# Performance work log

Hardware: AMD Instinct MI355X
Metric: run time of the kernel (lower is better)

## Reference

```python
import jax, jax.numpy as jnp
import numpy as np

B, C, D = 16384, 512, 512
EXT = 2
H = C * EXT
TAU = 1.0          # temperature_train
STEP = 0.05        # langevin_step_size
NOISE = 0.1        # langevin_noise
STEPS = 32         # langevin_steps


def setup_inputs() -> dict:
    key = jax.random.key(0)
    ks = jax.random.split(key, 8)
    s_in = 1.0 / np.sqrt(D)
    s_h = 1.0 / np.sqrt(H)
    return {
        'x': jax.random.normal(ks[0], (B, D), jnp.float32),
        'vanilla_components': jnp.abs(jax.random.normal(ks[1], (C, D), jnp.float32) * 0.1),
        'e_sp': jax.random.normal(ks[2], (C * D,), jnp.float32) * 0.1,
        'W1e': jax.random.normal(ks[3], (D, H), jnp.float32) * s_in,
        'b1e': jnp.zeros((H,), jnp.float32),
        'W2e': jax.random.normal(ks[4], (H, C), jnp.float32) * s_h,
        'b2e': jnp.zeros((C,), jnp.float32),
        'W1r': jax.random.normal(ks[5], (D, H), jnp.float32) * s_in,
        'b1r': jnp.zeros((H,), jnp.float32),
        'W2r': jax.random.normal(ks[6], (H, C), jnp.float32) * s_h,
        'b2r': jnp.zeros((C,), jnp.float32),
    }


def _langevin_gate(e, key):
    """Langevin MCMC on latent u with quadratic energy E(u)=0.5||u||^2 + <e,u>.
    Returns selection probability sigmoid(-u/tau)."""
    def step(u, k):
        grad = u + e  # dE/du
        u = u - STEP * grad + NOISE * jax.random.normal(k, u.shape, u.dtype)
        return u, None
    u, _ = jax.lax.scan(step, jnp.zeros_like(e), jax.random.split(key, STEPS))
    return jax.nn.sigmoid(-u / TAU)


def reference(x, vanilla_components, e_sp, W1e, b1e, W2e, b2e, W1r, b1r, W2r, b2r):
    k1, k2 = jax.random.split(jax.random.key(42))
    # non-negative components
    comps = jnp.abs(vanilla_components)  # [C, D]
    # fixed energy-based sparsity mask over component entries
    p_sp = _langevin_gate(e_sp, k1).reshape(C, D)
    comps = comps * p_sp
    # dynamic per-sample component selection energies via MLP
    h = jax.nn.relu(x @ W1e + b1e)          # [B, H]
    e_dyn = h @ W2e + b2e                   # [B, C]
    gate = _langevin_gate(e_dyn, k2)        # [B, C] soft gates (train mode)
    hr = jax.nn.relu(x @ W1r + b1r)         # [B, H]
    conc = (hr @ W2r + b2r) * gate          # [B, C]
    # aggregate: (concentration * components).sum over components -> [B, D]
    return conc @ comps
```

## Files before the change

kernel.cpp:

```cpp
#include <hip/hip_runtime.h>
#include <hip/hip_bf16.h>
#include <stdint.h>

#define Bn 16384
#define Cn 512
#define Dn 512
#define Hn 1024

#define A32 0.80628851f

typedef __attribute__((ext_vector_type(8))) short bf16x8;
typedef __attribute__((ext_vector_type(4))) float f32x4;
typedef __attribute__((ext_vector_type(2))) float f32x2;

__device__ __forceinline__ ushort f2bf(float f) {
  uint32_t u = __float_as_uint(f);
  return (ushort)((u + 0x7fffu + ((u >> 16) & 1u)) >> 16);
}
__device__ __forceinline__ float b2f(ushort u) {
  return __uint_as_float((uint32_t)u << 16);
}

typedef __attribute__((address_space(3))) uint32_t lds_u32_t;
typedef const __attribute__((address_space(1))) uint32_t glb_u32_t;
__device__ __forceinline__ void gload16(const ushort* g, ushort* l) {
  __builtin_amdgcn_global_load_lds((glb_u32_t*)g, (lds_u32_t*)l, 16, 0, 0);
}

constexpr uint32_t crotl(uint32_t v, int s) {
  return (v << s) | (v >> (32 - s));
}
struct TFOut { uint32_t w0, w1; };
constexpr TFOut ctf(uint32_t k0, uint32_t k1, uint32_t x0, uint32_t x1) {
  const uint32_t ks[3] = {k0, k1, k0 ^ k1 ^ 0x1BD11BDAu};
  const int rot[8] = {13, 15, 26, 6, 17, 29, 16, 24};
  uint32_t a = x0 + k0, b = x1 + k1;
  for (int g = 0; g < 5; ++g) {
    for (int i = 0; i < 4; ++i) {
      int r = rot[(g & 1) * 4 + i];
      a += b; b = crotl(b, r); b ^= a;
    }
    a += ks[(g + 1) % 3];
    b += ks[(g + 2) % 3] + (uint32_t)(g + 1);
  }
  return {a, b};
}
struct KeySched { uint32_t s[64]; uint32_t d[64]; };
constexpr KeySched make_keys() {
  KeySched K{};
  TFOut k1 = ctf(0u, 42u, 0u, 0u);
  TFOut k2 = ctf(0u, 42u, 0u, 1u);
  for (uint32_t t = 0; t < 32; ++t) {
    TFOut ws = ctf(k1.w0, k1.w1, 0u, t);
    K.s[2 * t] = ws.w0; K.s[2 * t + 1] = ws.w1;
    TFOut wd = ctf(k2.w0, k2.w1, 0u, t);
    K.d[2 * t] = wd.w0; K.d[2 * t + 1] = wd.w1;
  }
  return K;
}
__constant__ KeySched KS = make_keys();

__device__ __forceinline__ uint32_t rotl32(uint32_t v, int s) {
  return __builtin_rotateleft32(v, (uint32_t)s);
}
__device__ __forceinline__ uint32_t tf_xor(uint32_t K0, uint32_t K1,
                                           uint32_t KX, uint32_t j) {
  uint32_t a = K0, b = K1 + j;
#define TR(r) { a += b; b = rotl32(b, (r)); b ^= a; }
  TR(13) TR(15) TR(26) TR(6)   a += K1; b += KX + 1u;
  TR(17) TR(29) TR(16) TR(24)  a += KX; b += K0 + 2u;
  TR(13) TR(15) TR(26) TR(6)   a += K0; b += K1 + 3u;
  TR(17) TR(29) TR(16) TR(24)  a += K1; b += KX + 4u;
  TR(13) TR(15) TR(26) TR(6)   a += KX; b += K0 + 5u;
#undef TR
  return a ^ b;
}

__device__ __forceinline__ float bits_to_normal(uint32_t bits) {
  float f = __uint_as_float((bits >> 9) | 0x3f800000u) - 1.0f;
  float x = f * 2.0f - 0x1.fffffep-1f;
  float w = -__logf(1.0f - x * x);
  float p;
  if (w < 5.0f) {
    w -= 2.5f;
    p =            2.81022636e-08f;
    p = fmaf(p, w, 3.43273939e-07f);
    p = fmaf(p, w, -3.5233877e-06f);
    p = fmaf(p, w, -4.39150654e-06f);
    p = fmaf(p, w, 0.00021858087f);
    p = fmaf(p, w, -0.00125372503f);
    p = fmaf(p, w, -0.00417768164f);
    p = fmaf(p, w, 0.246640727f);
    p = fmaf(p, w, 1.50140941f);
  } else {
    w = sqrtf(w) - 3.0f;
    p =            -0.000200214257f;
    p = fmaf(p, w, 0.000100950558f);
    p = fmaf(p, w, 0.00134934322f);
    p = fmaf(p, w, -0.00367342844f);
    p = fmaf(p, w, 0.00573950773f);
    p = fmaf(p, w, -0.0076224613f);
    p = fmaf(p, w, 0.00943887047f);
    p = fmaf(p, w, 1.00167406f);
    p = fmaf(p, w, 2.83297682f);
  }
  return 0x1.6a09e6p+0f * (p * x);
}

__device__ __forceinline__ void z_block(ushort* __restrict__ Z, uint32_t zidx) {
  const uint32_t j0 = (zidx * 256u + threadIdx.x) * 2u;
  const uint32_t j1 = j0 + 1u;
  float z0 = 0.0f, z1 = 0.0f;
#pragma unroll 4
  for (int t = 0; t < 32; ++t) {
    const uint32_t K0 = KS.d[2 * t], K1 = KS.d[2 * t + 1];
    const uint32_t KX = K0 ^ K1 ^ 0x1BD11BDAu;
    uint32_t a0 = K0, b0 = K1 + j0;
    uint32_t a1 = K0, b1 = K1 + j1;
#define R2(r)                                                  \
    a0 += b0; a1 += b1;                                        \
    b0 = rotl32(b0, (r)); b1 = rotl32(b1, (r));                \
    b0 ^= a0; b1 ^= a1;
#define I2(p, q) a0 += (p); a1 += (p); b0 += (q); b1 += (q);
    R2(13) R2(15) R2(26) R2(6)  I2(K1, KX + 1u)
    R2(17) R2(29) R2(16) R2(24) I2(KX, K0 + 2u)
    R2(13) R2(15) R2(26) R2(6)  I2(K0, K1 + 3u)
    R2(17) R2(29) R2(16) R2(24) I2(K1, KX + 4u)
    R2(13) R2(15) R2(26) R2(6)  I2(KX, K0 + 5u)
#undef R2
#undef I2
    uint32_t s0 = a0 ^ b0, s1 = a1 ^ b1;
    float f0 = __uint_as_float((s0 >> 9) | 0x3f800000u) - 1.0f;
    float f1 = __uint_as_float((s1 >> 9) | 0x3f800000u) - 1.0f;
    float x0 = f0 * 2.0f - 0x1.fffffep-1f;
    float x1 = f1 * 2.0f - 0x1.fffffep-1f;
    float w0 = fminf(-__logf(fmaf(-x0, x0, 1.0f)), 5.0f) - 2.5f;
    float w1 = fminf(-__logf(fmaf(-x1, x1, 1.0f)), 5.0f) - 2.5f;
    f32x2 X = {x0, x1}, W = {w0, w1};
    f32x2 P = {2.81022636e-08f, 2.81022636e-08f};
    P = __builtin_elementwise_fma(P, W, (f32x2){3.43273939e-07f, 3.43273939e-07f});
    P = __builtin_elementwise_fma(P, W, (f32x2){-3.5233877e-06f, -3.5233877e-06f});
    P = __builtin_elementwise_fma(P, W, (f32x2){-4.39150654e-06f, -4.39150654e-06f});
    P = __builtin_elementwise_fma(P, W, (f32x2){0.00021858087f, 0.00021858087f});
    P = __builtin_elementwise_fma(P, W, (f32x2){-0.00125372503f, -0.00125372503f});
    P = __builtin_elementwise_fma(P, W, (f32x2){-0.00417768164f, -0.00417768164f});
    P = __builtin_elementwise_fma(P, W, (f32x2){0.246640727f, 0.246640727f});
    P = __builtin_elementwise_fma(P, W, (f32x2){1.50140941f, 1.50140941f});
    f32x2 Q = (P * X) * (f32x2){0.14142135f, 0.14142135f};
    z0 = fmaf(0.95f, z0, Q.x);
    z1 = fmaf(0.95f, z1, Q.y);
  }
  *(ushort2*)(Z + j0) = make_ushort2(f2bf(z0), f2bf(z1));
}

__device__ __forceinline__ void transpose_tile(
    const float* __restrict__ in, ushort* __restrict__ out,
    int N, int K, int tIdx, float T[32][33]) {
  const int ntn = N / 32;
  const int tk = tIdx / ntn, tn = tIdx % ntn;
  const int tx = threadIdx.x & 31, ty = threadIdx.x >> 5;
  const int k0 = tk * 32, n0 = tn * 32;
#pragma unroll
  for (int r = 0; r < 32; r += 8)
    T[ty + r][tx] = in[(size_t)(k0 + ty + r) * N + n0 + tx];
  __syncthreads();
#pragma unroll
  for (int r = 0; r < 32; r += 8)
    out[(size_t)(n0 + ty + r) * K + k0 + tx] = f2bf(T[tx][ty + r]);
}

__device__ __forceinline__ void smask_block(
    const float* __restrict__ vc, const float* __restrict__ e_sp,
    ushort* __restrict__ compsT, int g) {
  uint32_t jj = (uint32_t)g * 256 + threadIdx.x;
  uint32_t c = jj & (Cn - 1), d = jj >> 9;
  uint32_t ridx = c * Dn + d;
  float e = e_sp[ridx];
  float u = 0.0f;
#pragma unroll 4
  for (int t = 0; t < 32; ++t) {
    const uint32_t K0 = KS.s[2 * t], K1 = KS.s[2 * t + 1];
    uint32_t s = tf_xor(K0, K1, K0 ^ K1 ^ 0x1BD11BDAu, ridx);
    float n = bits_to_normal(s);
    u = (u - 0.05f * (u + e)) + 0.1f * n;
  }
  float gt = 1.0f / (1.0f + __expf(u));
  compsT[jj] = f2bf(fabsf(vc[ridx]) * gt);
}

__global__ __launch_bounds__(256) void k_prep_z(
    const float* __restrict__ x, ushort* __restrict__ x_bf,
    const float* __restrict__ W1e, ushort* __restrict__ W1eT,
    const float* __restrict__ W2e, ushort* __restrict__ W2eT,
    const float* __restrict__ W1r, ushort* __restrict__ W1rT,
    const float* __restrict__ W2r, ushort* __restrict__ W2rT,
    const float* __restrict__ vc, const float* __restrict__ e_sp,
    ushort* __restrict__ compsT, ushort* __restrict__ Zd) {
  __shared__ float T[32][33];
  const int pos = blockIdx.x;
  if ((pos % 5) == 4) {
    z_block(Zd, (uint32_t)(pos / 5));
    return;
  }
  const int p = (pos / 5) * 4 + (pos % 5);
  if (p < 8192) {
    int i = (p * 256 + threadIdx.x) * 4;
    float4 v = *(const float4*)(x + i);
    *(ushort4*)(x_bf + i) =
        make_ushort4(f2bf(v.x), f2bf(v.y), f2bf(v.z), f2bf(v.w));
  } else if (p < 8704) {
    transpose_tile(W1e, W1eT, Hn, Dn, p - 8192, T);
  } else if (p < 9216) {
    transpose_tile(W2e, W2eT, Cn, Hn, p - 8704, T);
  } else if (p < 9728) {
    transpose_tile(W1r, W1rT, Hn, Dn, p - 9216, T);
  } else if (p < 10240) {
    transpose_tile(W2r, W2rT, Cn, Hn, p - 9728, T);
  } else {
    smask_block(vc, e_sp, compsT, p - 10240);
  }
}

__device__ __forceinline__ void gemm_core(
    const ushort* __restrict__ A, const ushort* __restrict__ WT,
    int m0, int n0, int LD, int K,
    ushort* __restrict__ AsL, ushort* __restrict__ BsL,
    f32x4 acc[4][4]) {
  const int t = threadIdx.x;
  const int wave = t >> 6, lane = t & 63;
  const int row = t >> 2;
  const int col8 = ((t & 3) << 3) ^ (((t >> 3) & 3) << 3);
  const int wm = (wave >> 1) << 6, wn = (wave & 1) << 6;
  const int quad = lane >> 4, l15 = lane & 15;
  const int rc = (quad << 3) ^ (((l15 >> 1) & 3) << 3);

  const ushort* ga0 = A  + (size_t)(m0 + row) * LD + col8;
  const ushort* ga1 = A  + (size_t)(m0 + 64 + row) * LD + col8;
  const ushort* gb0 = WT + (size_t)(n0 + row) * LD + col8;
  const ushort* gb1 = WT + (size_t)(n0 + 64 + row) * LD + col8;
  ushort* la0 = AsL + wave * 512;
  ushort* la1 = AsL + 2048 + wave * 512;
  ushort* lb0 = BsL + wave * 512;
  ushort* lb1 = BsL + 2048 + wave * 512;

  for (int k0 = 0; k0 < K; k0 += 32) {
    gload16(ga0 + k0, la0);
    gload16(ga1 + k0, la1);
    gload16(gb0 + k0, lb0);
    gload16(gb1 + k0, lb1);
    __syncthreads();
    bf16x8 af[4], bfr[4];
#pragma unroll
    for (int i = 0; i < 4; ++i) {
      af[i]  = *(const bf16x8*)&AsL[(wm + i * 16 + l15) * 32 + rc];
      bfr[i] = *(const bf16x8*)&BsL[(wn + i * 16 + l15) * 32 + rc];
    }
#pragma unroll
    for (int i = 0; i < 4; ++i)
#pragma unroll
      for (int j = 0; j < 4; ++j)
        acc[i][j] = __builtin_amdgcn_mfma_f32_16x16x32_bf16(af[i], bfr[j],
                                                            acc[i][j], 0, 0, 0);
    __syncthreads();
  }
}

__device__ __forceinline__ void gemm_tile_bf(
    const ushort* __restrict__ A, const ushort* __restrict__ WT,
    const float* __restrict__ bias, ushort* __restrict__ Out, int g,
    ushort* AsL, ushort* BsL) {
  const int n0 = (g & 7) * 128, m0 = (g >> 3) * 128;
  const int t = threadIdx.x;
  const int wave = t >> 6, lane = t & 63;
  const int wm = (wave >> 1) << 6, wn = (wave & 1) << 6;
  const int quad = lane >> 4, l15 = lane & 15;
  f32x4 acc[4][4] = {};
  gemm_core(A, WT, m0, n0, Dn, Dn, AsL, BsL, acc);
#pragma unroll
  for (int i = 0; i < 4; ++i)
#pragma unroll
    for (int j = 0; j < 4; ++j) {
      const int col = n0 + wn + j * 16 + l15;
      const float bv = bias[col];
#pragma unroll
      for (int r = 0; r < 4; ++r) {
        const int row = m0 + wm + i * 16 + quad * 4 + r;
        Out[(size_t)row * Hn + col] = f2bf(fmaxf(acc[i][j][r] + bv, 0.0f));
      }
    }
}

__global__ __launch_bounds__(256) void k_g13_z(
    const ushort* __restrict__ x_bf,
    const ushort* __restrict__ W1eT, const float* __restrict__ b1e,
    ushort* __restrict__ h,
    const ushort* __restrict__ W1rT, const float* __restrict__ b1r,
    ushort* __restrict__ hr, ushort* __restrict__ Zd) {
  __shared__ ushort AsL[4096];
  __shared__ ushort BsL[4096];
  const int pos = blockIdx.x;
  if (pos % 3) {
    z_block(Zd, 2816u + (uint32_t)(pos / 3) * 2u + (uint32_t)(pos % 3) - 1u);
    return;
  }
  const int gg = pos / 3;
  const int g = gg >> 1;
  if (gg & 1)
    gemm_tile_bf(x_bf, W1rT, b1r, hr, g, AsL, BsL);
  else
    gemm_tile_bf(x_bf, W1eT, b1e, h, g, AsL, BsL);
}

__device__ __forceinline__ void gemm_tile_f32out(
    const ushort* __restrict__ A, const ushort* __restrict__ WT,
    const float* __restrict__ bias, float* __restrict__ Out,
    int m0, int n0, ushort* AsL, ushort* BsL) {
  const int t = threadIdx.x;
  const int wave = t >> 6, lane = t & 63;
  const int wm = (wave >> 1) << 6, wn = (wave & 1) << 6;
  const int quad = lane >> 4, l15 = lane & 15;
  f32x4 acc[4][4] = {};
  gemm_core(A, WT, m0, n0, Hn, Hn, AsL, BsL, acc);
#pragma unroll
  for (int i = 0; i < 4; ++i)
#pragma unroll
    for (int j = 0; j < 4; ++j) {
      const int col = n0 + wn + j * 16 + l15;
      const float bv = bias[col];
#pragma unroll
      for (int r = 0; r < 4; ++r) {
        const int row = m0 + wm + i * 16 + quad * 4 + r;
        Out[(size_t)row * Cn + col] = acc[i][j][r] + bv;
      }
    }
}

__global__ __launch_bounds__(256) void k_e_z(
    const ushort* __restrict__ h, const ushort* __restrict__ W2eT,
    const float* __restrict__ b2e, float* __restrict__ e_out,
    ushort* __restrict__ Zd) {
  __shared__ ushort AsL[4096];
  __shared__ ushort BsL[4096];
  const int pos = blockIdx.x;
  if ((pos % 10) == 0) {
    const int tg = pos / 10;
    gemm_tile_f32out(h, W2eT, b2e, e_out, (tg >> 2) * 128, (tg & 3) * 128,
                     AsL, BsL);
  } else {
    z_block(Zd, 6912u + (uint32_t)(pos / 10) * 9u + (uint32_t)(pos % 10) - 1u);
  }
}

__global__ __launch_bounds__(256) void k_r_z(
    const ushort* __restrict__ hr, const ushort* __restrict__ W2rT,
    const float* __restrict__ b2r, float* __restrict__ cr_out,
    ushort* __restrict__ Zd) {
  __shared__ ushort AsL[4096];
  __shared__ ushort BsL[4096];
  const int pos = blockIdx.x;
  if (pos >= 5120) {
    z_block(Zd, 16128u + (uint32_t)(pos - 5120));
    return;
  }
  if ((pos % 10) == 0) {
    const int tg = pos / 10;
    gemm_tile_f32out(hr, W2rT, b2r, cr_out, (tg >> 2) * 128, (tg & 3) * 128,
                     AsL, BsL);
  } else {
    z_block(Zd, 11520u + (uint32_t)(pos / 10) * 9u + (uint32_t)(pos % 10) - 1u);
  }
}

__global__ __launch_bounds__(256) void k_gate(
    const float* __restrict__ e, const float* __restrict__ cr,
    ushort* __restrict__ Z) {
  const size_t i = ((size_t)blockIdx.x * 256u + threadIdx.x) * 8u;
  uint4 zv = *(const uint4*)(Z + i);
  ushort zs[8];
  *(uint4*)zs = zv;
  float ee[8], cc[8];
  *(float4*)(ee)     = *(const float4*)(e + i);
  *(float4*)(ee + 4) = *(const float4*)(e + i + 4);
  *(float4*)(cc)     = *(const float4*)(cr + i);
  *(float4*)(cc + 4) = *(const float4*)(cr + i + 4);
  ushort os[8];
#pragma unroll
  for (int k = 0; k < 8; ++k) {
    float z = b2f(zs[k]);
    float g = 1.0f / (1.0f + __expf(z - A32 * ee[k]));
    os[k] = f2bf(cc[k] * g);
  }
  *(uint4*)(Z + i) = *(uint4*)os;
}

__global__ __launch_bounds__(256) void k_gemm_out(
    const ushort* __restrict__ A, const ushort* __restrict__ WT,
    float* __restrict__ Out) {
  __shared__ ushort AsL[4096];
  __shared__ ushort BsL[4096];
  const int t = threadIdx.x;
  const int m0 = blockIdx.y * 128, n0 = blockIdx.x * 128;
  const int wave = t >> 6, lane = t & 63;
  const int wm = (wave >> 1) << 6, wn = (wave & 1) << 6;
  const int quad = lane >> 4, l15 = lane & 15;
  f32x4 acc[4][4] = {};
  gemm_core(A, WT, m0, n0, Cn, Cn, AsL, BsL, acc);
#pragma unroll
  for (int i = 0; i < 4; ++i)
#pragma unroll
    for (int j = 0; j < 4; ++j) {
      const int col = n0 + wn + j * 16 + l15;
#pragma unroll
      for (int r = 0; r < 4; ++r) {
        const int row = m0 + wm + i * 16 + quad * 4 + r;
        Out[(size_t)row * Dn + col] = acc[i][j][r];
      }
    }
}

extern "C" void kernel_launch(void* const* d_in, const int* in_sizes, int n_in,
                              void* d_out, int out_size, void* d_ws, size_t ws_size,
                              hipStream_t stream) {
  const float* x    = (const float*)d_in[0];
  const float* vc   = (const float*)d_in[1];
  const float* e_sp = (const float*)d_in[2];
  const float* W1e  = (const float*)d_in[3];
  const float* b1e  = (const float*)d_in[4];
  const float* W2e  = (const float*)d_in[5];
  const float* b2e  = (const float*)d_in[6];
  const float* W1r  = (const float*)d_in[7];
  const float* b1r  = (const float*)d_in[8];
  const float* W2r  = (const float*)d_in[9];
  const float* b2r  = (const float*)d_in[10];
  float* out = (float*)d_out;

  char* ws = (char*)d_ws;
  ushort* W1eT   = (ushort*)(ws + (1u << 12));
  ushort* W2eT   = (ushort*)(ws + (1u << 12) + (1u << 20));
  ushort* W1rT   = (ushort*)(ws + (1u << 12) + (2u << 20));
  ushort* W2rT   = (ushort*)(ws + (1u << 12) + (3u << 20));
  ushort* compsT = (ushort*)(ws + (1u << 12) + (4u << 20));
  ushort* Zdyn   = (ushort*)(ws + (8u << 20));
  ushort* h_bf   = (ushort*)(ws + (24u << 20));
  ushort* hr_bf  = (ushort*)(ws + (56u << 20));
  float*  cr_f32 = (float*)(ws + (24u << 20));
  ushort* x_bf   = (ushort*)d_out;
  float*  e_f32  = (float*)d_out;

  k_prep_z<<<14080, 256, 0, stream>>>(x, x_bf, W1e, W1eT, W2e, W2eT,
                                      W1r, W1rT, W2r, W2rT, vc, e_sp, compsT,
                                      Zdyn);
  k_g13_z<<<6144, 256, 0, stream>>>(x_bf, W1eT, b1e, h_bf, W1rT, b1r, hr_bf,
                                    Zdyn);
  k_e_z<<<5120, 256, 0, stream>>>(h_bf, W2eT, b2e, e_f32, Zdyn);
  k_r_z<<<5376, 256, 0, stream>>>(hr_bf, W2rT, b2r, cr_f32, Zdyn);
  k_gate<<<4096, 256, 0, stream>>>(e_f32, cr_f32, Zdyn);
  k_gemm_out<<<dim3(Dn / 128, Bn / 128), 256, 0, stream>>>(Zdyn, compsT, out);
}
```

Before: 791.8 us.

## Double-buffer LDS tiles in shared GEMM core to overlap loads with MFMA

Rewrites the GEMM main loop to use two LDS buffers per operand. The next K-slice is issued via direct global-to-LDS loads while MFMAs run on the current one, with explicit vmcnt waits and barriers replacing the single-buffer load/sync/compute/sync pattern. This is meant to hide global load latency in all four GEMM kernels. In exchange LDS per block doubles to 32KB, which may lower occupancy, and correctness now depends on the hand-written waitcnt ordering.

```diff
diff --git a/kernel.cpp b/kernel.cpp
--- a/kernel.cpp
+++ b/kernel.cpp
@@ -221,10 +221,38 @@
   }
 }
 
+__device__ __forceinline__ void stage4(
+    const ushort* ga0, const ushort* ga1,
+    const ushort* gb0, const ushort* gb1,
+    int k, ushort* As, ushort* Bs, int wo) {
+  gload16(ga0 + k, As + wo);
+  gload16(ga1 + k, As + 2048 + wo);
+  gload16(gb0 + k, Bs + wo);
+  gload16(gb1 + k, Bs + 2048 + wo);
+}
+
+__device__ __forceinline__ void mfma16(
+    const ushort* Ac, const ushort* Bc,
+    int wm, int wn, int l15, int rc, f32x4 acc[4][4]) {
+  bf16x8 af[4], bfr[4];
+#pragma unroll
+  for (int i = 0; i < 4; ++i) {
+    af[i]  = *(const bf16x8*)&Ac[(wm + i * 16 + l15) * 32 + rc];
+    bfr[i] = *(const bf16x8*)&Bc[(wn + i * 16 + l15) * 32 + rc];
+  }
+#pragma unroll
+  for (int i = 0; i < 4; ++i)
+#pragma unroll
+    for (int j = 0; j < 4; ++j)
+      acc[i][j] = __builtin_amdgcn_mfma_f32_16x16x32_bf16(af[i], bfr[j],
+                                                          acc[i][j], 0, 0, 0);
+}
+
 __device__ __forceinline__ void gemm_core(
     const ushort* __restrict__ A, const ushort* __restrict__ WT,
     int m0, int n0, int LD, int K,
-    ushort* __restrict__ AsL, ushort* __restrict__ BsL,
+    ushort* __restrict__ As0, ushort* __restrict__ Bs0,
+    ushort* __restrict__ As1, ushort* __restrict__ Bs1,
     f32x4 acc[4][4]) {
   const int t = threadIdx.x;
   const int wave = t >> 6, lane = t & 63;
@@ -233,49 +261,46 @@
   const int wm = (wave >> 1) << 6, wn = (wave & 1) << 6;
   const int quad = lane >> 4, l15 = lane & 15;
   const int rc = (quad << 3) ^ (((l15 >> 1) & 3) << 3);
+  const int wo = wave * 512;
 
   const ushort* ga0 = A  + (size_t)(m0 + row) * LD + col8;
   const ushort* ga1 = A  + (size_t)(m0 + 64 + row) * LD + col8;
   const ushort* gb0 = WT + (size_t)(n0 + row) * LD + col8;
   const ushort* gb1 = WT + (size_t)(n0 + 64 + row) * LD + col8;
-  ushort* la0 = AsL + wave * 512;
-  ushort* la1 = AsL + 2048 + wave * 512;
-  ushort* lb0 = BsL + wave * 512;
-  ushort* lb1 = BsL + 2048 + wave * 512;
-
-  for (int k0 = 0; k0 < K; k0 += 32) {
-    gload16(ga0 + k0, la0);
-    gload16(ga1 + k0, la1);
-    gload16(gb0 + k0, lb0);
-    gload16(gb1 + k0, lb1);
-    __syncthreads();
-    bf16x8 af[4], bfr[4];
-#pragma unroll
-    for (int i = 0; i < 4; ++i) {
-      af[i]  = *(const bf16x8*)&AsL[(wm + i * 16 + l15) * 32 + rc];
-      bfr[i] = *(const bf16x8*)&BsL[(wn + i * 16 + l15) * 32 + rc];
+
+  stage4(ga0, ga1, gb0, gb1, 0, As0, Bs0, wo);
+
+  for (int k0 = 0; k0 < K; k0 += 64) {
+    stage4(ga0, ga1, gb0, gb1, k0 + 32, As1, Bs1, wo);
+    asm volatile("s_waitcnt vmcnt(4)" ::: "memory");
+    __builtin_amdgcn_sched_barrier(0);
+    __builtin_amdgcn_s_barrier();
+    mfma16(As0, Bs0, wm, wn, l15, rc, acc);
+    __builtin_amdgcn_s_barrier();
+    if (k0 + 64 < K) {
+      stage4(ga0, ga1, gb0, gb1, k0 + 64, As0, Bs0, wo);
+      asm volatile("s_waitcnt vmcnt(4)" ::: "memory");
+    } else {
+      asm volatile("s_waitcnt vmcnt(0)" ::: "memory");
     }
-#pragma unroll
-    for (int i = 0; i < 4; ++i)
-#pragma unroll
-      for (int j = 0; j < 4; ++j)
-        acc[i][j] = __builtin_amdgcn_mfma_f32_16x16x32_bf16(af[i], bfr[j],
-                                                            acc[i][j], 0, 0, 0);
-    __syncthreads();
+    __builtin_amdgcn_sched_barrier(0);
+    __builtin_amdgcn_s_barrier();
+    mfma16(As1, Bs1, wm, wn, l15, rc, acc);
+    __builtin_amdgcn_s_barrier();
   }
 }
 
 __device__ __forceinline__ void gemm_tile_bf(
     const ushort* __restrict__ A, const ushort* __restrict__ WT,
     const float* __restrict__ bias, ushort* __restrict__ Out, int g,
-    ushort* AsL, ushort* BsL) {
+    ushort* As0, ushort* Bs0, ushort* As1, ushort* Bs1) {
   const int n0 = (g & 7) * 128, m0 = (g >> 3) * 128;
   const int t = threadIdx.x;
   const int wave = t >> 6, lane = t & 63;
   const int wm = (wave >> 1) << 6, wn = (wave & 1) << 6;
   const int quad = lane >> 4, l15 = lane & 15;
   f32x4 acc[4][4] = {};
-  gemm_core(A, WT, m0, n0, Dn, Dn, AsL, BsL, acc);
+  gemm_core(A, WT, m0, n0, Dn, Dn, As0, Bs0, As1, Bs1, acc);
 #pragma unroll
   for (int i = 0; i < 4; ++i)
 #pragma unroll
@@ -296,8 +321,10 @@
     ushort* __restrict__ h,
     const ushort* __restrict__ W1rT, const float* __restrict__ b1r,
     ushort* __restrict__ hr, ushort* __restrict__ Zd) {
-  __shared__ ushort AsL[4096];
-  __shared__ ushort BsL[4096];
+  __shared__ ushort As0[4096];
+  __shared__ ushort Bs0[4096];
+  __shared__ ushort As1[4096];
+  __shared__ ushort Bs1[4096];
   const int pos = blockIdx.x;
   if (pos % 3) {
     z_block(Zd, 2816u + (uint32_t)(pos / 3) * 2u + (uint32_t)(pos % 3) - 1u);
@@ -306,21 +333,21 @@
   const int gg = pos / 3;
   const int g = gg >> 1;
   if (gg & 1)
-    gemm_tile_bf(x_bf, W1rT, b1r, hr, g, AsL, BsL);
+    gemm_tile_bf(x_bf, W1rT, b1r, hr, g, As0, Bs0, As1, Bs1);
   else
-    gemm_tile_bf(x_bf, W1eT, b1e, h, g, AsL, BsL);
+    gemm_tile_bf(x_bf, W1eT, b1e, h, g, As0, Bs0, As1, Bs1);
 }
 
 __device__ __forceinline__ void gemm_tile_f32out(
     const ushort* __restrict__ A, const ushort* __restrict__ WT,
     const float* __restrict__ bias, float* __restrict__ Out,
-    int m0, int n0, ushort* AsL, ushort* BsL) {
+    int m0, int n0, ushort* As0, ushort* Bs0, ushort* As1, ushort* Bs1) {
   const int t = threadIdx.x;
   const int wave = t >> 6, lane = t & 63;
   const int wm = (wave >> 1) << 6, wn = (wave & 1) << 6;
   const int quad = lane >> 4, l15 = lane & 15;
   f32x4 acc[4][4] = {};
-  gemm_core(A, WT, m0, n0, Hn, Hn, AsL, BsL, acc);
+  gemm_core(A, WT, m0, n0, Hn, Hn, As0, Bs0, As1, Bs1, acc);
 #pragma unroll
   for (int i = 0; i < 4; ++i)
 #pragma unroll
@@ -339,13 +366,15 @@
     const ushort* __restrict__ h, const ushort* __restrict__ W2eT,
     const float* __restrict__ b2e, float* __restrict__ e_out,
     ushort* __restrict__ Zd) {
-  __shared__ ushort AsL[4096];
-  __shared__ ushort BsL[4096];
+  __shared__ ushort As0[4096];
+  __shared__ ushort Bs0[4096];
+  __shared__ ushort As1[4096];
+  __shared__ ushort Bs1[4096];
   const int pos = blockIdx.x;
   if ((pos % 10) == 0) {
     const int tg = pos / 10;
     gemm_tile_f32out(h, W2eT, b2e, e_out, (tg >> 2) * 128, (tg & 3) * 128,
-                     AsL, BsL);
+                     As0, Bs0, As1, Bs1);
   } else {
     z_block(Zd, 6912u + (uint32_t)(pos / 10) * 9u + (uint32_t)(pos % 10) - 1u);
   }
@@ -355,8 +384,10 @@
     const ushort* __restrict__ hr, const ushort* __restrict__ W2rT,
     const float* __restrict__ b2r, float* __restrict__ cr_out,
     ushort* __restrict__ Zd) {
-  __shared__ ushort AsL[4096];
-  __shared__ ushort BsL[4096];
+  __shared__ ushort As0[4096];
+  __shared__ ushort Bs0[4096];
+  __shared__ ushort As1[4096];
+  __shared__ ushort Bs1[4096];
   const int pos = blockIdx.x;
   if (pos >= 5120) {
     z_block(Zd, 16128u + (uint32_t)(pos - 5120));
@@ -365,7 +396,7 @@
   if ((pos % 10) == 0) {
     const int tg = pos / 10;
     gemm_tile_f32out(hr, W2rT, b2r, cr_out, (tg >> 2) * 128, (tg & 3) * 128,
-                     AsL, BsL);
+                     As0, Bs0, As1, Bs1);
   } else {
     z_block(Zd, 11520u + (uint32_t)(pos / 10) * 9u + (uint32_t)(pos % 10) - 1u);
   }
@@ -396,15 +427,17 @@
 __global__ __launch_bounds__(256) void k_gemm_out(
     const ushort* __restrict__ A, const ushort* __restrict__ WT,
     float* __restrict__ Out) {
-  __shared__ ushort AsL[4096];
-  __shared__ ushort BsL[4096];
+  __shared__ ushort As0[4096];
+  __shared__ ushort Bs0[4096];
+  __shared__ ushort As1[4096];
+  __shared__ ushort Bs1[4096];
   const int t = threadIdx.x;
   const int m0 = blockIdx.y * 128, n0 = blockIdx.x * 128;
   const int wave = t >> 6, lane = t & 63;
   const int wm = (wave >> 1) << 6, wn = (wave & 1) << 6;
   const int quad = lane >> 4, l15 = lane & 15;
   f32x4 acc[4][4] = {};
-  gemm_core(A, WT, m0, n0, Cn, Cn, AsL, BsL, acc);
+  gemm_core(A, WT, m0, n0, Cn, Cn, As0, Bs0, As1, Bs1, acc);
 #pragma unroll
   for (int i = 0; i < 4; ++i)
 #pragma unroll
```

After: 777.5 us. No clear change (-1.8%).
